# Kernel optimization log

Measured on AMD Instinct MI355X. Metric: run time of the kernel, lower is better.

## Reference

```python
import jax, jax.numpy as jnp
import numpy as np

S = 95      # spatial cube size
B = 2       # batch (events)
C0 = 8      # init_conv_nplanes
C1 = 16     # planes after one downsample (inplanes*2)
K = 3       # kernel size (init conv, basic blocks, downsample)
STR = 2     # downsample stride
EPS = 1e-4  # scn BatchNorm eps
N = 40000   # total active voxels


def conv3d(x, w, stride, padding):
    # x: [B,D,H,W,Cin], w: [k,k,k,Cin,Cout]
    return jax.lax.conv_general_dilated(x, w, (stride,) * 3, padding,
                                        dimension_numbers=('NDHWC', 'DHWIO', 'NDHWC'))


def masked_bn(x, mask, gamma, beta, relu):
    # scn.BatchNorm(ReLU): per-channel stats over ACTIVE sites only
    n = jnp.maximum(mask.sum(), 1.0)
    mean = (x * mask).sum(axis=(0, 1, 2, 3)) / n
    var = (((x - mean) ** 2) * mask).sum(axis=(0, 1, 2, 3)) / n
    y = (x - mean) * jax.lax.rsqrt(var + EPS) * gamma + beta
    if relu:
        y = jnp.maximum(y, 0.0)
    return y * mask


def basic(x, mask, g1, b1, w1, g2, b2, w2):
    # pre-activation ResidualBlock_basic; submanifold convs keep the active-site mask
    y = masked_bn(x, mask, g1, b1, True)
    y = conv3d(y, w1, 1, 'SAME') * mask
    y = masked_bn(y, mask, g2, b2, True)
    y = conv3d(y, w2, 1, 'SAME') * mask
    return x + y


def downsample(x, mask, g1, b1, w1, g2, b2, w2, w3):
    # ResidualBlock_downsample: BNReLU -> {strided conv -> BNReLU -> submanifold conv} + {strided conv}
    y = masked_bn(x, mask, g1, b1, True)
    new_mask = jax.lax.reduce_window(mask, 0.0, jax.lax.max,
                                     (1, K, K, K, 1), (1, STR, STR, STR, 1), 'VALID')
    y1 = conv3d(y, w1, STR, 'VALID') * new_mask
    y1 = masked_bn(y1, new_mask, g2, b2, True)
    y1 = conv3d(y1, w2, 1, 'SAME') * new_mask
    y2 = conv3d(y, w3, STR, 'VALID') * new_mask
    return y1 + y2, new_mask


def _forward(coords, feats, w0, g0, b0,
             ba0_g1, ba0_b1, ba0_w1, ba0_g2, ba0_b2, ba0_w2,
             ba1_g1, ba1_b1, ba1_w1, ba1_g2, ba1_b2, ba1_w2,
             bo0_g1, bo0_b1, bo0_w1, bo0_g2, bo0_b2, bo0_w2,
             bo1_g1, bo1_b1, bo1_w1, bo1_g2, bo1_b2, bo1_w2,
             dn_g1, dn_b1, dn_w1, dn_g2, dn_b2, dn_w2, dn_w3,
             l1_w, l1_b, l2_w, l2_b):
    bi, xi, yi, zi = coords[:, 3], coords[:, 0], coords[:, 1], coords[:, 2]
    # scn.InputLayer: scatter (summing duplicates) into dense grid; inactive sites are exactly 0
    grid = jnp.zeros((B, S, S, S, 1), jnp.float32).at[bi, xi, yi, zi].add(feats)
    mask = jnp.zeros((B, S, S, S, 1), jnp.float32).at[bi, xi, yi, zi, 0].set(1.0)
    # ConvBNBlock: submanifold conv + BN + ReLU
    x = conv3d(grid, w0, 1, 'SAME') * mask
    x = masked_bn(x, mask, g0, b0, True)
    x = basic(x, mask, ba0_g1, ba0_b1, ba0_w1, ba0_g2, ba0_b2, ba0_w2)
    x = basic(x, mask, ba1_g1, ba1_b1, ba1_w1, ba1_g2, ba1_b2, ba1_w2)
    x, mask = downsample(x, mask, dn_g1, dn_b1, dn_w1, dn_g2, dn_b2, dn_w2, dn_w3)
    x = basic(x, mask, bo0_g1, bo0_b1, bo0_w1, bo0_g2, bo0_b2, bo0_w2)
    x = basic(x, mask, bo1_g1, bo1_b1, bo1_w1, bo1_g2, bo1_b2, bo1_w2)
    # scn.MaxPooling(full size, stride 1) + SparseToDense + squeeze: max over active sites -> [B, C1]
    pooled = jnp.where(mask > 0, x, -jnp.inf).max(axis=(1, 2, 3))
    pooled = jnp.where(jnp.isfinite(pooled), pooled, 0.0)
    h = pooled @ l1_w.T + l1_b
    return h @ l2_w.T + l2_b


def setup_inputs():
    keys = iter(jax.random.split(jax.random.key(0), 64))
    xyz = jax.random.randint(next(keys), (N, 3), 0, S, dtype=jnp.int32)
    bidx = jax.random.randint(next(keys), (N, 1), 0, B, dtype=jnp.int32)
    coords = jnp.concatenate([xyz, bidx], axis=1)
    feats = jax.random.normal(next(keys), (N, 1), dtype=jnp.float32)

    def wconv(shape):
        fan = shape[0] * shape[1] * shape[2] * shape[3]
        return jax.random.normal(next(keys), shape, jnp.float32) / np.float32(np.sqrt(fan))

    def gamma(c):
        return 1.0 + 0.1 * jax.random.normal(next(keys), (c,), jnp.float32)

    def beta(c):
        return 0.1 * jax.random.normal(next(keys), (c,), jnp.float32)

    d = {'coords': coords, 'feats': feats}
    d['w0'] = wconv((K, K, K, 1, C0)); d['g0'] = gamma(C0); d['b0'] = beta(C0)
    for name, c in [('ba0', C0), ('ba1', C0), ('bo0', C1), ('bo1', C1)]:
        d[name + '_g1'] = gamma(c); d[name + '_b1'] = beta(c); d[name + '_w1'] = wconv((K, K, K, c, c))
        d[name + '_g2'] = gamma(c); d[name + '_b2'] = beta(c); d[name + '_w2'] = wconv((K, K, K, c, c))
    d['dn_g1'] = gamma(C0); d['dn_b1'] = beta(C0); d['dn_w1'] = wconv((K, K, K, C0, C1))
    d['dn_g2'] = gamma(C1); d['dn_b2'] = beta(C1); d['dn_w2'] = wconv((K, K, K, C1, C1))
    d['dn_w3'] = wconv((K, K, K, C0, C1))
    d['l1_w'] = jax.random.normal(next(keys), (32, C1), jnp.float32) / np.float32(np.sqrt(C1))
    d['l1_b'] = beta(32)
    d['l2_w'] = jax.random.normal(next(keys), (1, 32), jnp.float32) / np.float32(np.sqrt(32))
    d['l2_b'] = beta(1)
    return d


def reference(coords, feats, w0, g0, b0,
              ba0_g1, ba0_b1, ba0_w1, ba0_g2, ba0_b2, ba0_w2,
              ba1_g1, ba1_b1, ba1_w1, ba1_g2, ba1_b2, ba1_w2,
              bo0_g1, bo0_b1, bo0_w1, bo0_g2, bo0_b2, bo0_w2,
              bo1_g1, bo1_b1, bo1_w1, bo1_g2, bo1_b2, bo1_w2,
              dn_g1, dn_b1, dn_w1, dn_g2, dn_b2, dn_w2, dn_w3,
              l1_w, l1_b, l2_w, l2_b):
    return _forward(coords, feats, w0, g0, b0,
                    ba0_g1, ba0_b1, ba0_w1, ba0_g2, ba0_b2, ba0_w2,
                    ba1_g1, ba1_b1, ba1_w1, ba1_g2, ba1_b2, ba1_w2,
                    bo0_g1, bo0_b1, bo0_w1, bo0_g2, bo0_b2, bo0_w2,
                    bo1_g1, bo1_b1, bo1_w1, bo1_g2, bo1_b2, bo1_w2,
                    dn_g1, dn_b1, dn_w1, dn_g2, dn_b2, dn_w2, dn_w3,
                    l1_w, l1_b, l2_w, l2_b)
```

## Files before the change

### kernel.cpp

```cpp
#include <hip/hip_runtime.h>
#include <cmath>

constexpr int S    = 95;
constexpr int B    = 2;
constexpr int S3   = S * S * S;
constexpr int S1   = 47;
constexpr int S13  = S1 * S1 * S1;
constexpr int NPTS = 40000;
constexpr int C0   = 8;
constexpr int C1   = 16;
constexpr float EPS = 1e-4f;
constexpr double SSCALE     = 1048576.0;
constexpr double INV_SSCALE = 1.0 / 1048576.0;

__device__ __forceinline__ unsigned encf(float f) {
    unsigned b = __float_as_uint(f);
    return (b & 0x80000000u) ? ~b : (b | 0x80000000u);
}
__device__ __forceinline__ float decf(unsigned e) {
    unsigned b = (e & 0x80000000u) ? (e ^ 0x80000000u) : ~e;
    return __uint_as_float(b);
}

template <int COUT, int SPLIT, int NW>
__device__ __forceinline__ void stats_accum(const float* acc, bool valid,
                                            float* ls, unsigned long long* stat_out) {
    constexpr int CT = COUT / SPLIT;
    float s0[CT], s1[CT];
#pragma unroll
    for (int j = 0; j < CT; ++j) { float v = valid ? acc[j] : 0.f; s0[j] = v; s1[j] = v * v; }
#pragma unroll
    for (int off = SPLIT; off < 64; off <<= 1) {
#pragma unroll
        for (int j = 0; j < CT; ++j) {
            s0[j] += __shfl_xor(s0[j], off, 64);
            s1[j] += __shfl_xor(s1[j], off, 64);
        }
    }
    int tid = threadIdx.x, lane = tid & 63, wv = tid >> 6;
    if (lane < SPLIT) {
#pragma unroll
        for (int j = 0; j < CT; ++j) {
            ls[wv * 2 * COUT + lane * CT + j]        = s0[j];
            ls[wv * 2 * COUT + COUT + lane * CT + j] = s1[j];
        }
    }
    __syncthreads();
    if (tid < 2 * COUT) {
        float t = 0.f;
#pragma unroll
        for (int w = 0; w < NW; ++w) t += ls[w * 2 * COUT + tid];
        long long q = llrint((double)t * SSCALE);
        atomicAdd(&stat_out[tid], (unsigned long long)q);
    }
}

template <int COUT, int SPLIT, int NW>
__device__ __forceinline__ void stats_accum_w(const float* acc, bool valid, int gw0,
                                              float* ls, unsigned long long* stat_out) {
    constexpr int CT = COUT / SPLIT;
    float s0[CT], s1[CT];
#pragma unroll
    for (int j = 0; j < CT; ++j) { float v = valid ? acc[j] : 0.f; s0[j] = v; s1[j] = v * v; }
#pragma unroll
    for (int off = 1; off < 64; off <<= 1) {
#pragma unroll
        for (int j = 0; j < CT; ++j) {
            s0[j] += __shfl_xor(s0[j], off, 64);
            s1[j] += __shfl_xor(s1[j], off, 64);
        }
    }
    int tid = threadIdx.x, lane = tid & 63, wv = tid >> 6;
    if (lane == 0) {
#pragma unroll
        for (int j = 0; j < CT; ++j) {
            ls[wv * 2 * CT + j]      = s0[j];
            ls[wv * 2 * CT + CT + j] = s1[j];
        }
    }
    __syncthreads();
    if (tid < 2 * COUT) {
        int part = tid / COUT;
        int ch   = tid - part * COUT;
        int qc   = ch / CT, jj = ch - qc * CT;
        float t = 0.f;
#pragma unroll
        for (int w = 0; w < NW; ++w)
            if (((gw0 + w) % SPLIT) == qc) t += ls[w * 2 * CT + part * CT + jj];
        long long q = llrint((double)t * SSCALE);
        atomicAdd(&stat_out[tid], (unsigned long long)q);
    }
}

template <int C>
__device__ __forceinline__ void bn_prologue(const unsigned long long* stat_in,
                                            const float* gamma, const float* beta,
                                            const int* cnt_bn, float* s_sc, float* s_sh) {
    int tid = threadIdx.x;
    if (tid < C) {
        double n   = fmax((double)cnt_bn[0], 1.0);
        double sm  = (double)(long long)stat_in[tid] * INV_SSCALE;
        double ssq = (double)(long long)stat_in[C + tid] * INV_SSCALE;
        double mean = sm / n;
        double var  = ssq / n - mean * mean;
        float sc = gamma[tid] * rsqrtf((float)var + EPS);
        s_sc[tid] = sc;
        s_sh[tid] = fmaf(-(float)mean, sc, beta[tid]);
    }
}

__global__ __launch_bounds__(256) void k_scatter(const int* __restrict__ coords,
                                                 const float* __restrict__ feats,
                                                 float* __restrict__ grid, int* __restrict__ map0,
                                                 int* __restrict__ list0, int* __restrict__ cnt0) {
    int i = blockIdx.x * 256 + threadIdx.x;
    bool valid = i < NPTS;
    int v = 0; bool own = false;
    if (valid) {
        int x = coords[i * 4 + 0], y = coords[i * 4 + 1], z = coords[i * 4 + 2], b = coords[i * 4 + 3];
        v = ((b * S + x) * S + y) * S + z;
        atomicAdd(&grid[v], feats[i]);
        own = (atomicCAS(&map0[v], 0, -1) == 0);
    }
    unsigned long long m = __ballot(own);
    int lane = threadIdx.x & 63;
    int base = 0;
    if (lane == 0) { int cw = __popcll(m); if (cw) base = atomicAdd(cnt0, cw); }
    base = __shfl(base, 0, 64);
    if (own) {
        int pos = base + __popcll(m & ((1ull << lane) - 1ull));
        list0[pos] = v;
        map0[v] = pos + 1;
    }
}

__global__ __launch_bounds__(256) void k_conv0s(const float* __restrict__ grid,
                                                const int* __restrict__ list, const int* __restrict__ cnt,
                                                const float* __restrict__ w, float* __restrict__ out,
                                                unsigned long long* __restrict__ stat_out) {
    __shared__ float wl[27 * C0];
    __shared__ float ls[4 * 2 * C0];
    const int tid = threadIdx.x;
    if (tid < 27 * C0) wl[tid] = w[tid];
    __syncthreads();
    int i = blockIdx.x * 256 + tid;
    bool valid = i < cnt[0];
    float acc[C0];
#pragma unroll
    for (int c = 0; c < C0; ++c) acc[c] = 0.f;
    if (valid) {
        int v = list[i];
        int z = v % S; int t = v / S;
        int y = t % S; t /= S;
        int x = t % S; int b = t / S;
        float gg[27];
#pragma unroll
        for (int kx = 0; kx < 3; ++kx) {
            int xx = x + kx - 1;
#pragma unroll
            for (int ky = 0; ky < 3; ++ky) {
                int yy = y + ky - 1;
#pragma unroll
                for (int kz = 0; kz < 3; ++kz) {
                    int zz = z + kz - 1;
                    bool in = (unsigned)xx < (unsigned)S && (unsigned)yy < (unsigned)S && (unsigned)zz < (unsigned)S;
                    gg[(kx * 3 + ky) * 3 + kz] = in ? grid[((b * S + xx) * S + yy) * S + zz] : 0.f;
                }
            }
        }
#pragma unroll
        for (int tap = 0; tap < 27; ++tap) {
            float g = gg[tap];
            if (g != 0.f) {
#pragma unroll
                for (int c = 0; c < C0; ++c) acc[c] = fmaf(g, wl[tap * C0 + c], acc[c]);
            }
        }
    }
    stats_accum<C0, 1, 4>(acc, valid, ls, stat_out);
    if (valid) {
#pragma unroll
        for (int c = 0; c < C0; ++c) out[(size_t)i * C0 + c] = acc[c];
    }
}

__global__ __launch_bounds__(256) void k_bn0(float* __restrict__ xs, const int* __restrict__ cnt,
                                             const unsigned long long* __restrict__ stat_in,
                                             const float* __restrict__ gamma, const float* __restrict__ beta,
                                             unsigned long long* __restrict__ stat_out) {
    __shared__ float ls[4 * 2 * C0];
    __shared__ float s_sc[C0], s_sh[C0];
    bn_prologue<C0>(stat_in, gamma, beta, cnt, s_sc, s_sh);
    __syncthreads();
    int tid = threadIdx.x;
    int i = blockIdx.x * 256 + tid;
    bool valid = i < cnt[0];
    float vals[C0];
#pragma unroll
    for (int c = 0; c < C0; ++c) vals[c] = 0.f;
    if (valid) {
#pragma unroll
        for (int c = 0; c < C0; ++c)
            vals[c] = fmaxf(fmaf(xs[(size_t)i * C0 + c], s_sc[c], s_sh[c]), 0.f);
#pragma unroll
        for (int c = 0; c < C0; ++c) xs[(size_t)i * C0 + c] = vals[c];
    }
    stats_accum<C0, 1, 4>(vals, valid, ls, stat_out);
}

template <int CIN, int COUT, int SPLIT, int SGOUT, int STRIDE, int MODE, int TB>
__global__ __launch_bounds__(TB) void k_conv_f(const float* __restrict__ xs,
                                               const unsigned long long* __restrict__ stat_in,
                                               const float* __restrict__ gamma,
                                               const float* __restrict__ beta,
                                               const int* __restrict__ cnt_bn,
                                               const int* __restrict__ map,
                                               const int* __restrict__ list,
                                               const int* __restrict__ cnt,
                                               const float* __restrict__ w,
                                               const float* __restrict__ res,
                                               float* __restrict__ out,
                                               unsigned long long* __restrict__ stat_out,
                                               unsigned* __restrict__ pooled) {
    constexpr int SGIN = (STRIDE == 2) ? S : SGOUT;
    constexpr int CT = COUT / SPLIT;
    constexpr int NW = TB / 64;
    __shared__ float wl[27 * CIN * COUT];
    __shared__ float ls[NW * 2 * COUT];
    __shared__ float s_sc[CIN], s_sh[CIN];
    const int tid = threadIdx.x;
    const int n_act = cnt[0];
    bn_prologue<CIN>(stat_in, gamma, beta, cnt_bn, s_sc, s_sh);
    const bool blk_on = (int)(((long)blockIdx.x * TB) / SPLIT) < n_act;
    if (blk_on) {
        for (int idx = tid; idx < 27 * CIN * COUT; idx += TB) wl[idx] = w[idx];
    }
    __syncthreads();

    long gt = (long)blockIdx.x * TB + tid;
    int i = (int)(gt / SPLIT), q = (int)(gt % SPLIT);
    bool valid = i < n_act;

    float acc[CT];
#pragma unroll
    for (int j = 0; j < CT; ++j) acc[j] = 0.f;
    if (valid && res) {
#pragma unroll
        for (int j = 0; j < CT; ++j) acc[j] = res[(size_t)i * COUT + q * CT + j];
    }
    if (valid) {
        int v = list[i];
        int z = v % SGOUT; int t2 = v / SGOUT;
        int y = t2 % SGOUT; t2 /= SGOUT;
        int x = t2 % SGOUT; int b = t2 / SGOUT;
        int mm[27];
#pragma unroll
        for (int kx = 0; kx < 3; ++kx) {
            int xx = (STRIDE == 2) ? (2 * x + kx) : (x + kx - 1);
#pragma unroll
            for (int ky = 0; ky < 3; ++ky) {
                int yy = (STRIDE == 2) ? (2 * y + ky) : (y + ky - 1);
#pragma unroll
                for (int kz = 0; kz < 3; ++kz) {
                    int zz = (STRIDE == 2) ? (2 * z + kz) : (z + kz - 1);
                    bool in = (STRIDE == 2) ||
                              ((unsigned)xx < (unsigned)SGIN && (unsigned)yy < (unsigned)SGIN &&
                               (unsigned)zz < (unsigned)SGIN);
                    mm[(kx * 3 + ky) * 3 + kz] = in ? map[((b * SGIN + xx) * SGIN + yy) * SGIN + zz] : 0;
                }
            }
        }
#pragma unroll
        for (int tap = 0; tap < 27; ++tap) {
            int m = mm[tap];
            if (m > 0) {
                const float* row = &xs[(size_t)(m - 1) * CIN];
                float rv[CIN];
                const float4* r4 = reinterpret_cast<const float4*>(row);
#pragma unroll
                for (int u = 0; u < CIN / 4; ++u) {
                    float4 f = r4[u];
                    rv[4 * u] = f.x; rv[4 * u + 1] = f.y; rv[4 * u + 2] = f.z; rv[4 * u + 3] = f.w;
                }
                const float* wt = &wl[tap * CIN * COUT + q * CT];
#pragma unroll
                for (int ci = 0; ci < CIN; ++ci) {
                    float g = fmaxf(fmaf(rv[ci], s_sc[ci], s_sh[ci]), 0.f);
#pragma unroll
                    for (int j = 0; j < CT; ++j) acc[j] = fmaf(g, wt[ci * COUT + j], acc[j]);
                }
            }
        }
    }
    if (MODE == 1) stats_accum<COUT, SPLIT, NW>(acc, valid, ls, stat_out);
    if (valid) {
#pragma unroll
        for (int j = 0; j < CT; ++j) out[(size_t)i * COUT + q * CT + j] = acc[j];
    }
}

template <int CIN, int COUT, int SPLIT, int MODE, int TB>
__global__ __launch_bounds__(TB) void k_conv_w(const float* __restrict__ xs,
                                               const unsigned long long* __restrict__ stat_in,
                                               const float* __restrict__ gamma,
                                               const float* __restrict__ beta,
                                               const int* __restrict__ cnt_bn,
                                               const int* __restrict__ map,
                                               const int* __restrict__ list,
                                               const int* __restrict__ cnt,
                                               const float* __restrict__ w,
                                               const float* __restrict__ res,
                                               float* __restrict__ out,
                                               unsigned long long* __restrict__ stat_out,
                                               unsigned* __restrict__ pooled) {
    constexpr int CT = COUT / SPLIT;
    constexpr int NW = TB / 64;
    __shared__ float ls[NW * 2 * CT];
    __shared__ float s_sc[CIN], s_sh[CIN];
    __shared__ unsigned sm[B * COUT];
    const int tid  = threadIdx.x;
    const int lane = tid & 63;
    const int gw0  = blockIdx.x * NW;
    const int n_act = cnt[0];

    if (MODE == 2 && tid < B * COUT) sm[tid] = 0u;
    bn_prologue<CIN>(stat_in, gamma, beta, cnt_bn, s_sc, s_sh);
    __syncthreads();

    int gw = __builtin_amdgcn_readfirstlane(gw0 + (tid >> 6));
    int q  = gw % SPLIT;
    int c  = gw / SPLIT;
    int i  = c * 64 + lane;
    bool valid = i < n_act;

    float scr[CIN], shr[CIN];
#pragma unroll
    for (int ci = 0; ci < CIN; ++ci) { scr[ci] = s_sc[ci]; shr[ci] = s_sh[ci]; }

    float acc[CT];
#pragma unroll
    for (int j = 0; j < CT; ++j) acc[j] = 0.f;
    int b = 0;

    if (c * 64 < n_act) {
        if (valid && res) {
#pragma unroll
            for (int j = 0; j < CT; ++j) acc[j] = res[(size_t)i * COUT + q * CT + j];
        }
        int mm[27];
#pragma unroll
        for (int t = 0; t < 27; ++t) mm[t] = 0;
        if (valid) {
            int v = list[i];
            int z = v % S1; int t2 = v / S1;
            int y = t2 % S1; t2 /= S1;
            int x = t2 % S1; b = t2 / S1;
#pragma unroll
            for (int kx = 0; kx < 3; ++kx) {
                int xx = x + kx - 1;
#pragma unroll
                for (int ky = 0; ky < 3; ++ky) {
                    int yy = y + ky - 1;
#pragma unroll
                    for (int kz = 0; kz < 3; ++kz) {
                        int zz = z + kz - 1;
                        bool in = (unsigned)xx < (unsigned)S1 && (unsigned)yy < (unsigned)S1 &&
                                  (unsigned)zz < (unsigned)S1;
                        mm[(kx * 3 + ky) * 3 + kz] = in ? map[((b * S1 + xx) * S1 + yy) * S1 + zz] : 0;
                    }
                }
            }
        }
        const float* wq = w + q * CT;
        for (int tap = 0; tap < 27; ++tap) {
            int m = mm[tap];
            float rv[CIN];
            if (m > 0) {
                const float4* r4 = reinterpret_cast<const float4*>(&xs[(size_t)(m - 1) * CIN]);
#pragma unroll
                for (int u = 0; u < CIN / 4; ++u) {
                    float4 f = r4[u];
                    rv[4 * u] = f.x; rv[4 * u + 1] = f.y; rv[4 * u + 2] = f.z; rv[4 * u + 3] = f.w;
                }
            }
            const float* wt = wq + (size_t)tap * CIN * COUT;
#pragma unroll
            for (int ci = 0; ci < CIN; ++ci) {
                float g = fmaxf(fmaf(rv[ci], scr[ci], shr[ci]), 0.f);
                g = (m > 0) ? g : 0.f;
#pragma unroll
                for (int j = 0; j < CT; ++j)
                    acc[j] = fmaf(g, wt[ci * COUT + j], acc[j]);
            }
        }
    }

    if (MODE == 1) {
        stats_accum_w<COUT, SPLIT, NW>(acc, valid, gw0, ls, stat_out);
        if (valid) {
#pragma unroll
            for (int j = 0; j < CT; ++j) out[(size_t)i * COUT + q * CT + j] = acc[j];
        }
    } else {
        if (valid) {
#pragma unroll
            for (int j = 0; j < CT; ++j) atomicMax(&sm[b * COUT + q * CT + j], encf(acc[j]));
        }
        __syncthreads();
        if (tid < B * COUT) { unsigned e = sm[tid]; if (e) atomicMax(&pooled[tid], e); }
    }
}

template <int TB>
__global__ __launch_bounds__(TB) void k_conv_s2_dual(const float* __restrict__ xs,
                                                     const unsigned long long* __restrict__ stat_in,
                                                     const float* __restrict__ gamma,
                                                     const float* __restrict__ beta,
                                                     const int* __restrict__ cnt_bn,
                                                     const int* __restrict__ map0,
                                                     const int* __restrict__ list1,
                                                     const int* __restrict__ cnt1,
                                                     const float* __restrict__ w1,
                                                     const float* __restrict__ w3,
                                                     float* __restrict__ out1,
                                                     float* __restrict__ out3,
                                                     unsigned long long* __restrict__ stat_out) {
    constexpr int CIN = C0, COUT = C1, SPLIT = 2, CT = COUT / SPLIT;
    constexpr int NW = TB / 64;
    __shared__ float wl1[27 * CIN * COUT];
    __shared__ float wl3[27 * CIN * COUT];
    __shared__ float ls[NW * 2 * COUT];
    __shared__ float s_sc[CIN], s_sh[CIN];
    const int tid = threadIdx.x;
    const int n_act = cnt1[0];
    bn_prologue<CIN>(stat_in, gamma, beta, cnt_bn, s_sc, s_sh);
    const bool blk_on = (int)(((long)blockIdx.x * TB) / SPLIT) < n_act;
    if (blk_on) {
        for (int idx = tid; idx < 27 * CIN * COUT; idx += TB) { wl1[idx] = w1[idx]; wl3[idx] = w3[idx]; }
    }
    __syncthreads();

    long gt = (long)blockIdx.x * TB + tid;
    int i = (int)(gt / SPLIT), q = (int)(gt % SPLIT);
    bool valid = i < n_act;

    float acc1[CT], acc3[CT];
#pragma unroll
    for (int j = 0; j < CT; ++j) { acc1[j] = 0.f; acc3[j] = 0.f; }
    if (valid) {
        int v = list1[i];
        int z = v % S1; int t2 = v / S1;
        int y = t2 % S1; t2 /= S1;
        int x = t2 % S1; int b = t2 / S1;
        int mm[27];
#pragma unroll
        for (int kx = 0; kx < 3; ++kx) {
#pragma unroll
            for (int ky = 0; ky < 3; ++ky) {
#pragma unroll
                for (int kz = 0; kz < 3; ++kz) {
                    mm[(kx * 3 + ky) * 3 + kz] =
                        map0[((b * S + 2 * x + kx) * S + 2 * y + ky) * S + 2 * z + kz];
                }
            }
        }
#pragma unroll
        for (int tap = 0; tap < 27; ++tap) {
            int m = mm[tap];
            if (m > 0) {
                const float* row = &xs[(size_t)(m - 1) * CIN];
                float rv[CIN];
                const float4* r4 = reinterpret_cast<const float4*>(row);
#pragma unroll
                for (int u = 0; u < CIN / 4; ++u) {
                    float4 f = r4[u];
                    rv[4 * u] = f.x; rv[4 * u + 1] = f.y; rv[4 * u + 2] = f.z; rv[4 * u + 3] = f.w;
                }
                const float* wt1 = &wl1[tap * CIN * COUT + q * CT];
                const float* wt3 = &wl3[tap * CIN * COUT + q * CT];
#pragma unroll
                for (int ci = 0; ci < CIN; ++ci) {
                    float g = fmaxf(fmaf(rv[ci], s_sc[ci], s_sh[ci]), 0.f);
#pragma unroll
                    for (int j = 0; j < CT; ++j) {
                        acc1[j] = fmaf(g, wt1[ci * COUT + j], acc1[j]);
                        acc3[j] = fmaf(g, wt3[ci * COUT + j], acc3[j]);
                    }
                }
            }
        }
    }
    stats_accum<COUT, SPLIT, NW>(acc1, valid, ls, stat_out);
    if (valid) {
#pragma unroll
        for (int j = 0; j < CT; ++j) {
            out1[(size_t)i * COUT + q * CT + j] = acc1[j];
            out3[(size_t)i * COUT + q * CT + j] = acc3[j];
        }
    }
}

__global__ __launch_bounds__(256) void k_map1(const int* __restrict__ map0, int* __restrict__ map1,
                                              int* __restrict__ list1, int* __restrict__ cnt1) {
    int v = blockIdx.x * 256 + threadIdx.x;
    bool valid = v < B * S13;
    bool act = false;
    if (valid) {
        int z = v % S1; int t = v / S1;
        int y = t % S1; t /= S1;
        int x = t % S1; int b = t / S1;
#pragma unroll
        for (int kx = 0; kx < 3; ++kx)
#pragma unroll
            for (int ky = 0; ky < 3; ++ky)
#pragma unroll
                for (int kz = 0; kz < 3; ++kz) {
                    int n = ((b * S + 2 * x + kx) * S + 2 * y + ky) * S + 2 * z + kz;
                    act = act || (map0[n] != 0);
                }
    }
    __shared__ int s_w[4];
    unsigned long long bm = __ballot(act);
    int lane = threadIdx.x & 63, wv = threadIdx.x >> 6;
    int cw = __popcll(bm);
    if (lane == 0) s_w[wv] = cw;
    __syncthreads();
    if (threadIdx.x == 0) {
        int tot = s_w[0] + s_w[1] + s_w[2] + s_w[3];
        int base = tot ? atomicAdd(cnt1, tot) : 0;
        int a = base;
        for (int k = 0; k < 4; ++k) { int c = s_w[k]; s_w[k] = a; a += c; }
    }
    __syncthreads();
    if (valid) {
        if (act) {
            int pos = s_w[wv] + __popcll(bm & ((1ull << lane) - 1ull));
            list1[pos] = v;
            map1[v] = pos + 1;
        } else {
            map1[v] = 0;
        }
    }
}

__global__ __launch_bounds__(64) void k_head(const unsigned* __restrict__ pooled,
                                             const float* __restrict__ l1w, const float* __restrict__ l1b,
                                             const float* __restrict__ l2w, const float* __restrict__ l2b,
                                             float* __restrict__ outp) {
    int t = threadIdx.x;
    int b = t >> 5, j = t & 31;
    float h = l1b[j];
#pragma unroll
    for (int c = 0; c < C1; ++c) {
        unsigned e = pooled[b * C1 + c];
        float p = (e == 0u) ? 0.f : decf(e);
        h = fmaf(l1w[j * C1 + c], p, h);
    }
    float val = l2w[j] * h;
#pragma unroll
    for (int off = 16; off > 0; off >>= 1) val += __shfl_down(val, off, 32);
    if (j == 0) outp[b] = val + l2b[0];
}

extern "C" void kernel_launch(void* const* d_in, const int* in_sizes, int n_in,
                              void* d_out, int out_size, void* d_ws, size_t ws_size,
                              hipStream_t stream) {
    const int*   coords = (const int*)  d_in[0];
    const float* feats  = (const float*)d_in[1];
    const float* w0     = (const float*)d_in[2];
    const float* g0     = (const float*)d_in[3];
    const float* b0     = (const float*)d_in[4];
    const float* ba0_g1 = (const float*)d_in[5];
    const float* ba0_b1 = (const float*)d_in[6];
    const float* ba0_w1 = (const float*)d_in[7];
    const float* ba0_g2 = (const float*)d_in[8];
    const float* ba0_b2 = (const float*)d_in[9];
    const float* ba0_w2 = (const float*)d_in[10];
    const float* ba1_g1 = (const float*)d_in[11];
    const float* ba1_b1 = (const float*)d_in[12];
    const float* ba1_w1 = (const float*)d_in[13];
    const float* ba1_g2 = (const float*)d_in[14];
    const float* ba1_b2 = (const float*)d_in[15];
    const float* ba1_w2 = (const float*)d_in[16];
    const float* bo0_g1 = (const float*)d_in[17];
    const float* bo0_b1 = (const float*)d_in[18];
    const float* bo0_w1 = (const float*)d_in[19];
    const float* bo0_g2 = (const float*)d_in[20];
    const float* bo0_b2 = (const float*)d_in[21];
    const float* bo0_w2 = (const float*)d_in[22];
    const float* bo1_g1 = (const float*)d_in[23];
    const float* bo1_b1 = (const float*)d_in[24];
    const float* bo1_w1 = (const float*)d_in[25];
    const float* bo1_g2 = (const float*)d_in[26];
    const float* bo1_b2 = (const float*)d_in[27];
    const float* bo1_w2 = (const float*)d_in[28];
    const float* dn_g1  = (const float*)d_in[29];
    const float* dn_b1  = (const float*)d_in[30];
    const float* dn_w1  = (const float*)d_in[31];
    const float* dn_g2  = (const float*)d_in[32];
    const float* dn_b2  = (const float*)d_in[33];
    const float* dn_w2  = (const float*)d_in[34];
    const float* dn_w3  = (const float*)d_in[35];
    const float* l1_w   = (const float*)d_in[36];
    const float* l1_b   = (const float*)d_in[37];
    const float* l2_w   = (const float*)d_in[38];
    const float* l2_b   = (const float*)d_in[39];

    char* p = (char*)d_ws;
    auto take = [&](size_t elems) -> float* {
        float* r = (float*)p;
        p += ((elems * 4 + 255) / 256) * 256;
        return r;
    };
    float* grid    = take((size_t)B * S3);
    int*   map0    = (int*)take((size_t)B * S3);
    float* x0      = take((size_t)NPTS * C0);
    float* t0      = take((size_t)NPTS * C0);
    int*   map1    = (int*)take((size_t)B * S13);
    float* t1      = take((size_t)B * S13 * C1);
    float* r1      = take((size_t)B * S13 * C1);
    float* x1      = take((size_t)B * S13 * C1);
    unsigned long long* stats = (unsigned long long*)take(11 * 32 * 2);
    unsigned* pooled = (unsigned*)take(B * C1);
    int*   cnt     = (int*)take(16);
    char* zero_end = p;
    int*   list0   = (int*)take(NPTS);
    int*   list1   = (int*)take((size_t)B * S13);
    int* cnt0 = cnt;
    int* cnt1 = cnt + 1;
    auto G = [&](int g) { return stats + (size_t)g * 32; };

    hipMemsetAsync(grid, 0, (size_t)((char*)x0 - (char*)grid), stream);
    hipMemsetAsync(stats, 0, (size_t)(zero_end - (char*)stats), stream);

    constexpr int TB1 = 512;
    const int NB_C0 = (NPTS + 255) / 256;
    const int NB_L0 = (NPTS * 4 + 255) / 256;
    const int NB_M1 = (B * S13 + 255) / 256;
    const int NB_L1 = (B * S13 * 2 + TB1 - 1) / TB1;

    k_scatter<<<NB_C0, 256, 0, stream>>>(coords, feats, grid, map0, list0, cnt0);
    k_conv0s<<<NB_C0, 256, 0, stream>>>(grid, list0, cnt0, w0, x0, G(0));
    k_bn0<<<NB_C0, 256, 0, stream>>>(x0, cnt0, G(0), g0, b0, G(1));

    k_conv_f<C0, C0, 4, S, 1, 1, 256><<<NB_L0, 256, 0, stream>>>(x0, G(1), ba0_g1, ba0_b1, cnt0,
                                                                 map0, list0, cnt0, ba0_w1, nullptr, t0, G(2), nullptr);
    k_conv_f<C0, C0, 4, S, 1, 1, 256><<<NB_L0, 256, 0, stream>>>(t0, G(2), ba0_g2, ba0_b2, cnt0,
                                                                 map0, list0, cnt0, ba0_w2, x0, x0, G(3), nullptr);

    k_conv_f<C0, C0, 4, S, 1, 1, 256><<<NB_L0, 256, 0, stream>>>(x0, G(3), ba1_g1, ba1_b1, cnt0,
                                                                 map0, list0, cnt0, ba1_w1, nullptr, t0, G(4), nullptr);
    k_conv_f<C0, C0, 4, S, 1, 1, 256><<<NB_L0, 256, 0, stream>>>(t0, G(4), ba1_g2, ba1_b2, cnt0,
                                                                 map0, list0, cnt0, ba1_w2, x0, x0, G(5), nullptr);

    k_map1<<<NB_M1, 256, 0, stream>>>(map0, map1, list1, cnt1);
    k_conv_s2_dual<TB1><<<NB_L1, TB1, 0, stream>>>(x0, G(5), dn_g1, dn_b1, cnt0,
                                                   map0, list1, cnt1, dn_w1, dn_w3, t1, r1, G(6));
    k_conv_w<C1, C1, 2, 1, TB1><<<NB_L1, TB1, 0, stream>>>(t1, G(6), dn_g2, dn_b2, cnt1,
                                                           map1, list1, cnt1, dn_w2, r1, x1, G(7), nullptr);

    k_conv_w<C1, C1, 2, 1, TB1><<<NB_L1, TB1, 0, stream>>>(x1, G(7), bo0_g1, bo0_b1, cnt1,
                                                           map1, list1, cnt1, bo0_w1, nullptr, t1, G(8), nullptr);
    k_conv_w<C1, C1, 2, 1, TB1><<<NB_L1, TB1, 0, stream>>>(t1, G(8), bo0_g2, bo0_b2, cnt1,
                                                           map1, list1, cnt1, bo0_w2, x1, x1, G(9), nullptr);

    k_conv_w<C1, C1, 2, 1, TB1><<<NB_L1, TB1, 0, stream>>>(x1, G(9), bo1_g1, bo1_b1, cnt1,
                                                           map1, list1, cnt1, bo1_w1, nullptr, t1, G(10), nullptr);
    k_conv_w<C1, C1, 2, 2, TB1><<<NB_L1, TB1, 0, stream>>>(t1, G(10), bo1_g2, bo1_b2, cnt1,
                                                           map1, list1, cnt1, bo1_w2, x1, nullptr, nullptr, pooled);

    k_head<<<1, 64, 0, stream>>>(pooled, l1_w, l1_b, l2_w, l2_b, (float*)d_out);
}
```

Baseline: 400.5 us.

## Pad stat atomics, warp-split strided dual conv, wave-reduce max pooling

Statistics accumulators are now spaced 16 slots apart, so atomics on different channels no longer share a cache line. The strided dual conv is reworked so each wave owns 64 voxels and one quarter of the output channels. It reads weights straight from global memory instead of staging them in LDS, and the level-1 convs move from a split of 2 to a split of 4. The max-pooling epilogue now does a wave-level max reduction per batch before issuing atomics. The head also gains a guard against non-finite pooled values. Together these aim to cut atomic contention, LDS weight staging and per-thread work, at the cost of more launched threads and redundant map lookups.

```diff
diff --git a/kernel.cpp b/kernel.cpp
--- a/kernel.cpp
+++ b/kernel.cpp
@@ -12,6 +12,7 @@
 constexpr float EPS = 1e-4f;
 constexpr double SSCALE     = 1048576.0;
 constexpr double INV_SSCALE = 1.0 / 1048576.0;
+constexpr int STP = 16;
 
 __device__ __forceinline__ unsigned encf(float f) {
     unsigned b = __float_as_uint(f);
@@ -51,7 +52,7 @@
 #pragma unroll
         for (int w = 0; w < NW; ++w) t += ls[w * 2 * COUT + tid];
         long long q = llrint((double)t * SSCALE);
-        atomicAdd(&stat_out[tid], (unsigned long long)q);
+        atomicAdd(&stat_out[(size_t)tid * STP], (unsigned long long)q);
     }
 }
 
@@ -88,7 +89,7 @@
         for (int w = 0; w < NW; ++w)
             if (((gw0 + w) % SPLIT) == qc) t += ls[w * 2 * CT + part * CT + jj];
         long long q = llrint((double)t * SSCALE);
-        atomicAdd(&stat_out[tid], (unsigned long long)q);
+        atomicAdd(&stat_out[(size_t)tid * STP], (unsigned long long)q);
     }
 }
 
@@ -99,8 +100,8 @@
     int tid = threadIdx.x;
     if (tid < C) {
         double n   = fmax((double)cnt_bn[0], 1.0);
-        double sm  = (double)(long long)stat_in[tid] * INV_SSCALE;
-        double ssq = (double)(long long)stat_in[C + tid] * INV_SSCALE;
+        double sm  = (double)(long long)stat_in[(size_t)tid * STP] * INV_SSCALE;
+        double ssq = (double)(long long)stat_in[(size_t)(C + tid) * STP] * INV_SSCALE;
         double mean = sm / n;
         double var  = ssq / n - mean * mean;
         float sc = gamma[tid] * rsqrtf((float)var + EPS);
@@ -208,7 +209,7 @@
     stats_accum<C0, 1, 4>(vals, valid, ls, stat_out);
 }
 
-template <int CIN, int COUT, int SPLIT, int SGOUT, int STRIDE, int MODE, int TB>
+template <int CIN, int COUT, int SPLIT, int SGOUT, int MODE, int TB>
 __global__ __launch_bounds__(TB) void k_conv_f(const float* __restrict__ xs,
                                                const unsigned long long* __restrict__ stat_in,
                                                const float* __restrict__ gamma,
@@ -222,7 +223,6 @@
                                                float* __restrict__ out,
                                                unsigned long long* __restrict__ stat_out,
                                                unsigned* __restrict__ pooled) {
-    constexpr int SGIN = (STRIDE == 2) ? S : SGOUT;
     constexpr int CT = COUT / SPLIT;
     constexpr int NW = TB / 64;
     __shared__ float wl[27 * CIN * COUT];
@@ -256,17 +256,16 @@
         int mm[27];
 #pragma unroll
         for (int kx = 0; kx < 3; ++kx) {
-            int xx = (STRIDE == 2) ? (2 * x + kx) : (x + kx - 1);
+            int xx = x + kx - 1;
 #pragma unroll
             for (int ky = 0; ky < 3; ++ky) {
-                int yy = (STRIDE == 2) ? (2 * y + ky) : (y + ky - 1);
+                int yy = y + ky - 1;
 #pragma unroll
                 for (int kz = 0; kz < 3; ++kz) {
-                    int zz = (STRIDE == 2) ? (2 * z + kz) : (z + kz - 1);
-                    bool in = (STRIDE == 2) ||
-                              ((unsigned)xx < (unsigned)SGIN && (unsigned)yy < (unsigned)SGIN &&
-                               (unsigned)zz < (unsigned)SGIN);
-                    mm[(kx * 3 + ky) * 3 + kz] = in ? map[((b * SGIN + xx) * SGIN + yy) * SGIN + zz] : 0;
+                    int zz = z + kz - 1;
+                    bool in = ((unsigned)xx < (unsigned)SGOUT && (unsigned)yy < (unsigned)SGOUT &&
+                               (unsigned)zz < (unsigned)SGOUT);
+                    mm[(kx * 3 + ky) * 3 + kz] = in ? map[((b * SGOUT + xx) * SGOUT + yy) * SGOUT + zz] : 0;
                 }
             }
         }
@@ -402,16 +401,27 @@
             for (int j = 0; j < CT; ++j) out[(size_t)i * COUT + q * CT + j] = acc[j];
         }
     } else {
-        if (valid) {
-#pragma unroll
-            for (int j = 0; j < CT; ++j) atomicMax(&sm[b * COUT + q * CT + j], encf(acc[j]));
+#pragma unroll
+        for (int bb = 0; bb < B; ++bb) {
+            float vv[CT];
+#pragma unroll
+            for (int j = 0; j < CT; ++j) vv[j] = (valid && b == bb) ? acc[j] : -INFINITY;
+#pragma unroll
+            for (int off = 1; off < 64; off <<= 1) {
+#pragma unroll
+                for (int j = 0; j < CT; ++j) vv[j] = fmaxf(vv[j], __shfl_xor(vv[j], off, 64));
+            }
+            if (lane == 0) {
+#pragma unroll
+                for (int j = 0; j < CT; ++j) atomicMax(&sm[bb * COUT + q * CT + j], encf(vv[j]));
+            }
         }
         __syncthreads();
         if (tid < B * COUT) { unsigned e = sm[tid]; if (e) atomicMax(&pooled[tid], e); }
     }
 }
 
-template <int TB>
+template <int SPLIT, int TB>
 __global__ __launch_bounds__(TB) void k_conv_s2_dual(const float* __restrict__ xs,
                                                      const unsigned long long* __restrict__ stat_in,
                                                      const float* __restrict__ gamma,
@@ -425,72 +435,77 @@
                                                      float* __restrict__ out1,
                                                      float* __restrict__ out3,
                                                      unsigned long long* __restrict__ stat_out) {
-    constexpr int CIN = C0, COUT = C1, SPLIT = 2, CT = COUT / SPLIT;
+    constexpr int CIN = C0, COUT = C1, CT = COUT / SPLIT;
     constexpr int NW = TB / 64;
-    __shared__ float wl1[27 * CIN * COUT];
-    __shared__ float wl3[27 * CIN * COUT];
-    __shared__ float ls[NW * 2 * COUT];
+    __shared__ float ls[NW * 2 * CT];
     __shared__ float s_sc[CIN], s_sh[CIN];
-    const int tid = threadIdx.x;
+    const int tid  = threadIdx.x;
+    const int lane = tid & 63;
+    const int gw0  = blockIdx.x * NW;
     const int n_act = cnt1[0];
     bn_prologue<CIN>(stat_in, gamma, beta, cnt_bn, s_sc, s_sh);
-    const bool blk_on = (int)(((long)blockIdx.x * TB) / SPLIT) < n_act;
-    if (blk_on) {
-        for (int idx = tid; idx < 27 * CIN * COUT; idx += TB) { wl1[idx] = w1[idx]; wl3[idx] = w3[idx]; }
-    }
-    __syncthreads();
-
-    long gt = (long)blockIdx.x * TB + tid;
-    int i = (int)(gt / SPLIT), q = (int)(gt % SPLIT);
+    __syncthreads();
+
+    int gw = __builtin_amdgcn_readfirstlane(gw0 + (tid >> 6));
+    int q  = gw % SPLIT;
+    int c  = gw / SPLIT;
+    int i  = c * 64 + lane;
     bool valid = i < n_act;
 
+    float scr[CIN], shr[CIN];
+#pragma unroll
+    for (int ci = 0; ci < CIN; ++ci) { scr[ci] = s_sc[ci]; shr[ci] = s_sh[ci]; }
+
     float acc1[CT], acc3[CT];
 #pragma unroll
     for (int j = 0; j < CT; ++j) { acc1[j] = 0.f; acc3[j] = 0.f; }
-    if (valid) {
-        int v = list1[i];
-        int z = v % S1; int t2 = v / S1;
-        int y = t2 % S1; t2 /= S1;
-        int x = t2 % S1; int b = t2 / S1;
+
+    if (c * 64 < n_act) {
         int mm[27];
 #pragma unroll
-        for (int kx = 0; kx < 3; ++kx) {
-#pragma unroll
-            for (int ky = 0; ky < 3; ++ky) {
-#pragma unroll
-                for (int kz = 0; kz < 3; ++kz) {
-                    mm[(kx * 3 + ky) * 3 + kz] =
-                        map0[((b * S + 2 * x + kx) * S + 2 * y + ky) * S + 2 * z + kz];
-                }
-            }
-        }
-#pragma unroll
+        for (int t = 0; t < 27; ++t) mm[t] = 0;
+        if (valid) {
+            int v = list1[i];
+            int z = v % S1; int t2 = v / S1;
+            int y = t2 % S1; t2 /= S1;
+            int x = t2 % S1; int b = t2 / S1;
+#pragma unroll
+            for (int kx = 0; kx < 3; ++kx)
+#pragma unroll
+                for (int ky = 0; ky < 3; ++ky)
+#pragma unroll
+                    for (int kz = 0; kz < 3; ++kz)
+                        mm[(kx * 3 + ky) * 3 + kz] =
+                            map0[((b * S + 2 * x + kx) * S + 2 * y + ky) * S + 2 * z + kz];
+        }
+        const float* wq1 = w1 + q * CT;
+        const float* wq3 = w3 + q * CT;
         for (int tap = 0; tap < 27; ++tap) {
             int m = mm[tap];
+            float rv[CIN];
             if (m > 0) {
-                const float* row = &xs[(size_t)(m - 1) * CIN];
-                float rv[CIN];
-                const float4* r4 = reinterpret_cast<const float4*>(row);
-#pragma unroll
-                for (int u = 0; u < CIN / 4; ++u) {
-                    float4 f = r4[u];
-                    rv[4 * u] = f.x; rv[4 * u + 1] = f.y; rv[4 * u + 2] = f.z; rv[4 * u + 3] = f.w;
-                }
-                const float* wt1 = &wl1[tap * CIN * COUT + q * CT];
-                const float* wt3 = &wl3[tap * CIN * COUT + q * CT];
-#pragma unroll
-                for (int ci = 0; ci < CIN; ++ci) {
-                    float g = fmaxf(fmaf(rv[ci], s_sc[ci], s_sh[ci]), 0.f);
-#pragma unroll
-                    for (int j = 0; j < CT; ++j) {
-                        acc1[j] = fmaf(g, wt1[ci * COUT + j], acc1[j]);
-                        acc3[j] = fmaf(g, wt3[ci * COUT + j], acc3[j]);
-                    }
-                }
-            }
-        }
-    }
-    stats_accum<COUT, SPLIT, NW>(acc1, valid, ls, stat_out);
+                const float2* r2 = reinterpret_cast<const float2*>(&xs[(size_t)(m - 1) * CIN]);
+#pragma unroll
+                for (int u = 0; u < CIN / 2; ++u) {
+                    float2 f = r2[u];
+                    rv[2 * u] = f.x; rv[2 * u + 1] = f.y;
+                }
+            }
+            const float* wt1 = wq1 + (size_t)tap * CIN * COUT;
+            const float* wt3 = wq3 + (size_t)tap * CIN * COUT;
+#pragma unroll
+            for (int ci = 0; ci < CIN; ++ci) {
+                float g = fmaxf(fmaf(rv[ci], scr[ci], shr[ci]), 0.f);
+                g = (m > 0) ? g : 0.f;
+#pragma unroll
+                for (int j = 0; j < CT; ++j) {
+                    acc1[j] = fmaf(g, wt1[ci * COUT + j], acc1[j]);
+                    acc3[j] = fmaf(g, wt3[ci * COUT + j], acc3[j]);
+                }
+            }
+        }
+    }
+    stats_accum_w<COUT, SPLIT, NW>(acc1, valid, gw0, ls, stat_out);
     if (valid) {
 #pragma unroll
         for (int j = 0; j < CT; ++j) {
@@ -554,6 +569,7 @@
     for (int c = 0; c < C1; ++c) {
         unsigned e = pooled[b * C1 + c];
         float p = (e == 0u) ? 0.f : decf(e);
+        p = isfinite(p) ? p : 0.f;
         h = fmaf(l1w[j * C1 + c], p, h);
     }
     float val = l2w[j] * h;
@@ -620,7 +636,7 @@
     float* t1      = take((size_t)B * S13 * C1);
     float* r1      = take((size_t)B * S13 * C1);
     float* x1      = take((size_t)B * S13 * C1);
-    unsigned long long* stats = (unsigned long long*)take(11 * 32 * 2);
+    unsigned long long* stats = (unsigned long long*)take(11 * 32 * STP * 2);
     unsigned* pooled = (unsigned*)take(B * C1);
     int*   cnt     = (int*)take(16);
     char* zero_end = p;
@@ -628,46 +644,47 @@
     int*   list1   = (int*)take((size_t)B * S13);
     int* cnt0 = cnt;
     int* cnt1 = cnt + 1;
-    auto G = [&](int g) { return stats + (size_t)g * 32; };
+    auto G = [&](int g) { return stats + (size_t)g * 32 * STP; };
 
     hipMemsetAsync(grid, 0, (size_t)((char*)x0 - (char*)grid), stream);
     hipMemsetAsync(stats, 0, (size_t)(zero_end - (char*)stats), stream);
 
     constexpr int TB1 = 512;
+    constexpr int SPL = 4;
     const int NB_C0 = (NPTS + 255) / 256;
     const int NB_L0 = (NPTS * 4 + 255) / 256;
     const int NB_M1 = (B * S13 + 255) / 256;
-    const int NB_L1 = (B * S13 * 2 + TB1 - 1) / TB1;
+    const int NB_W  = (B * S13 * SPL + TB1 - 1) / TB1;
 
     k_scatter<<<NB_C0, 256, 0, stream>>>(coords, feats, grid, map0, list0, cnt0);
     k_conv0s<<<NB_C0, 256, 0, stream>>>(grid, list0, cnt0, w0, x0, G(0));
     k_bn0<<<NB_C0, 256, 0, stream>>>(x0, cnt0, G(0), g0, b0, G(1));
 
-    k_conv_f<C0, C0, 4, S, 1, 1, 256><<<NB_L0, 256, 0, stream>>>(x0, G(1), ba0_g1, ba0_b1, cnt0,
-                                                                 map0, list0, cnt0, ba0_w1, nullptr, t0, G(2), nullptr);
-    k_conv_f<C0, C0, 4, S, 1, 1, 256><<<NB_L0, 256, 0, stream>>>(t0, G(2), ba0_g2, ba0_b2, cnt0,
-                                                                 map0, list0, cnt0, ba0_w2, x0, x0, G(3), nullptr);
-
-    k_conv_f<C0, C0, 4, S, 1, 1, 256><<<NB_L0, 256, 0, stream>>>(x0, G(3), ba1_g1, ba1_b1, cnt0,
-                                                                 map0, list0, cnt0, ba1_w1, nullptr, t0, G(4), nullptr);
-    k_conv_f<C0, C0, 4, S, 1, 1, 256><<<NB_L0, 256, 0, stream>>>(t0, G(4), ba1_g2, ba1_b2, cnt0,
-                                                                 map0, list0, cnt0, ba1_w2, x0, x0, G(5), nullptr);
+    k_conv_f<C0, C0, 4, S, 1, 256><<<NB_L0, 256, 0, stream>>>(x0, G(1), ba0_g1, ba0_b1, cnt0,
+                                                              map0, list0, cnt0, ba0_w1, nullptr, t0, G(2), nullptr);
+    k_conv_f<C0, C0, 4, S, 1, 256><<<NB_L0, 256, 0, stream>>>(t0, G(2), ba0_g2, ba0_b2, cnt0,
+                                                              map0, list0, cnt0, ba0_w2, x0, x0, G(3), nullptr);
+
+    k_conv_f<C0, C0, 4, S, 1, 256><<<NB_L0, 256, 0, stream>>>(x0, G(3), ba1_g1, ba1_b1, cnt0,
+                                                              map0, list0, cnt0, ba1_w1, nullptr, t0, G(4), nullptr);
+    k_conv_f<C0, C0, 4, S, 1, 256><<<NB_L0, 256, 0, stream>>>(t0, G(4), ba1_g2, ba1_b2, cnt0,
+                                                              map0, list0, cnt0, ba1_w2, x0, x0, G(5), nullptr);
 
     k_map1<<<NB_M1, 256, 0, stream>>>(map0, map1, list1, cnt1);
-    k_conv_s2_dual<TB1><<<NB_L1, TB1, 0, stream>>>(x0, G(5), dn_g1, dn_b1, cnt0,
-                                                   map0, list1, cnt1, dn_w1, dn_w3, t1, r1, G(6));
-    k_conv_w<C1, C1, 2, 1, TB1><<<NB_L1, TB1, 0, stream>>>(t1, G(6), dn_g2, dn_b2, cnt1,
-                                                           map1, list1, cnt1, dn_w2, r1, x1, G(7), nullptr);
-
-    k_conv_w<C1, C1, 2, 1, TB1><<<NB_L1, TB1, 0, stream>>>(x1, G(7), bo0_g1, bo0_b1, cnt1,
-                                                           map1, list1, cnt1, bo0_w1, nullptr, t1, G(8), nullptr);
-    k_conv_w<C1, C1, 2, 1, TB1><<<NB_L1, TB1, 0, stream>>>(t1, G(8), bo0_g2, bo0_b2, cnt1,
-                                                           map1, list1, cnt1, bo0_w2, x1, x1, G(9), nullptr);
-
-    k_conv_w<C1, C1, 2, 1, TB1><<<NB_L1, TB1, 0, stream>>>(x1, G(9), bo1_g1, bo1_b1, cnt1,
-                                                           map1, list1, cnt1, bo1_w1, nullptr, t1, G(10), nullptr);
-    k_conv_w<C1, C1, 2, 2, TB1><<<NB_L1, TB1, 0, stream>>>(t1, G(10), bo1_g2, bo1_b2, cnt1,
-                                                           map1, list1, cnt1, bo1_w2, x1, nullptr, nullptr, pooled);
+    k_conv_s2_dual<SPL, TB1><<<NB_W, TB1, 0, stream>>>(x0, G(5), dn_g1, dn_b1, cnt0,
+                                                       map0, list1, cnt1, dn_w1, dn_w3, t1, r1, G(6));
+    k_conv_w<C1, C1, SPL, 1, TB1><<<NB_W, TB1, 0, stream>>>(t1, G(6), dn_g2, dn_b2, cnt1,
+                                                            map1, list1, cnt1, dn_w2, r1, x1, G(7), nullptr);
+
+    k_conv_w<C1, C1, SPL, 1, TB1><<<NB_W, TB1, 0, stream>>>(x1, G(7), bo0_g1, bo0_b1, cnt1,
+                                                            map1, list1, cnt1, bo0_w1, nullptr, t1, G(8), nullptr);
+    k_conv_w<C1, C1, SPL, 1, TB1><<<NB_W, TB1, 0, stream>>>(t1, G(8), bo0_g2, bo0_b2, cnt1,
+                                                            map1, list1, cnt1, bo0_w2, x1, x1, G(9), nullptr);
+
+    k_conv_w<C1, C1, SPL, 1, TB1><<<NB_W, TB1, 0, stream>>>(x1, G(9), bo1_g1, bo1_b1, cnt1,
+                                                            map1, list1, cnt1, bo1_w1, nullptr, t1, G(10), nullptr);
+    k_conv_w<C1, C1, SPL, 2, TB1><<<NB_W, TB1, 0, stream>>>(t1, G(10), bo1_g2, bo1_b2, cnt1,
+                                                            map1, list1, cnt1, bo1_w2, x1, nullptr, nullptr, pooled);
 
     k_head<<<1, 64, 0, stream>>>(pooled, l1_w, l1_b, l2_w, l2_b, (float*)d_out);
 }
```

New measurement: 464.2 us. 1.16x slower.
